# Optimization experiments

Hardware: AMD Instinct MI355X
Metric: run time of the kernel (lower is better)

The kernel has to match this reference:

```python
import jax, jax.numpy as jnp
import numpy as np

PS = 2      # patch_size
TOPK = 3    # topk


def setup_inputs() -> dict:
    key = jax.random.key(0)
    x = jax.random.normal(key, (8, 128, 64, 64), dtype=jnp.float32)
    alpha = jnp.asarray(5.0, dtype=jnp.float32)  # nn.Parameter alpha
    return {"x": x, "alpha": alpha}


def _forward(x, alpha):
    ps = PS
    b, c, h, w = x.shape
    nph, npw = h // ps, w // ps
    npatch = nph * npw
    pa = ps * ps
    # F.normalize(p=2, dim=-3) with torch eps=1e-12
    norm = jnp.maximum(jnp.sqrt(jnp.sum(x * x, axis=1, keepdims=True)), 1e-12)
    x = x / norm
    # patchify -> [b, c, npatch, patch_area] (patches h-major, pixels row-major)
    xp = x.reshape(b, c, nph, ps, npw, ps).transpose(0, 1, 2, 4, 3, 5)
    xp = xp.reshape(b, c, npatch, pa)
    diag_idx = jnp.arange(ps) * (ps + 1)  # [0, 3] for ps=2
    # gather diagonal pixels of each patch -> [b, ps, npatch, c]
    xd = xp[:, :, :, diag_idx].transpose(0, 3, 2, 1)
    # patch correlation matmul -> [b, ps, npatch, npatch]
    corr = jnp.einsum('bpnc,bpmc->bpnm', xd, xd)
    avg = jnp.mean(corr, axis=1, keepdims=True)
    s = jnp.concatenate([corr, avg], axis=1)  # [b, ps+1, npatch, npatch]
    # ZeroWindow gaussian mask (rat_s=0.05); channel index = patch center (r,c)
    sr, sc = 0.05 * nph, 0.05 * npw
    rr = jnp.arange(nph, dtype=jnp.float32)
    cc = jnp.arange(npw, dtype=jnp.float32)
    cent_r, cent_c = jnp.meshgrid(rr, cc, indexing='ij')
    cent_r = cent_r.reshape(npatch)
    cent_c = cent_c.reshape(npatch)
    gr = jnp.exp(-(rr[None, :] - cent_r[:, None]) ** 2 / (2.0 * sr * sr))  # [npatch, nph]
    gc = jnp.exp(-(cc[None, :] - cent_c[:, None]) ** 2 / (2.0 * sc * sc))  # [npatch, npw]
    mask = (1.0 - gr[:, :, None] * gc[:, None, :]).reshape(npatch, npatch)
    s = s * mask[None, None]
    a = s * alpha
    # double (row + col) softmax
    s = jax.nn.softmax(a, axis=-1) * jax.nn.softmax(a, axis=-2)
    # expand avg channel to all patch pixels, scatter diagonal channels back
    new_x = jnp.broadcast_to(s[:, -1:], (b, pa, npatch, npatch))
    new_x = new_x.at[:, diag_idx].set(s[:, :ps])
    # un-patchify second npatch axis to spatial [b, npatch, h, w]
    y = jnp.swapaxes(new_x, 1, 3)  # [b, npatch, npatch, pa]
    y = y.reshape(b, npatch, nph, npw, ps, ps).transpose(0, 1, 2, 4, 3, 5)
    y = y.reshape(b, npatch, h, w)
    # topk over the npatch axis (dim=-3)
    vals = jax.lax.top_k(jnp.moveaxis(y, 1, -1), TOPK)[0]  # [b, h, w, k]
    return jnp.moveaxis(vals, -1, 1)  # [b, k, h, w]


def reference(x, alpha):
    return _forward(x, alpha)
```

## Files before the change

### kernel.cpp

```cpp
#include <hip/hip_runtime.h>
#include <hip/hip_bf16.h>
#include <math.h>

#define NB 8
#define NC 128
#define NH 64
#define NW 64
#define NP 1024
#define TWO_SIG2 5.12f

static const size_t CORR_OFF_B = 0;
static const size_t XD_OFF_B   = (size_t)NB * 2 * NP * NP * 4;
static const size_t RSUM_OFF_B = XD_OFF_B + (size_t)NB * 2 * NP * NC * 2;

typedef __bf16 bf16x8 __attribute__((ext_vector_type(8)));
typedef float f32x4 __attribute__((ext_vector_type(4)));

__device__ __forceinline__ int iabs_(int v) { return v < 0 ? -v : v; }

#define INSERT3(v, A, Bq, Cq)                \
  {                                          \
    const float _c1 = fminf(A, (v));         \
    A = fmaxf(A, (v));                       \
    const float _c2 = fminf(Bq, _c1);        \
    Bq = fmaxf(Bq, _c1);                     \
    Cq = fmaxf(Cq, _c2);                     \
  }

#define MERGE3(a0, a1, a2, b0, b1, b2)       \
  {                                          \
    const float _x1 = fmaxf(a0, b0);         \
    const float _y1 = fminf(a0, b0);         \
    const float _x2 = fmaxf(a1, b1);         \
    const float _z  = fmaxf(a2, b2);         \
    a0 = _x1;                                \
    a1 = fmaxf(_y1, _x2);                    \
    a2 = fmaxf(fminf(_y1, _x2), _z);         \
  }

__global__ __launch_bounds__(256) void k1_norm(const float* __restrict__ x,
                                               __hip_bfloat16* __restrict__ xd) {
  __shared__ __align__(16) float tile[NC * 65];
  const int chunk = blockIdx.x;
  const int p = blockIdx.y;
  const int b = blockIdx.z;
  const int t = threadIdx.x;
  const int pix = t & 63;
  const int cw = t >> 6;
  const int nbase = chunk * 64;

  {
    const int n = nbase + pix;
    const int i = ((n >> 5) << 1) + p;
    const int j = ((n & 31) << 1) + p;
    const float* xb = x + (size_t)b * NC * NH * NW + (size_t)i * NW + j;
    for (int cc = 0; cc < 32; ++cc) {
      const int c = (cc << 2) + cw;
      tile[c * 65 + pix] = xb[(size_t)c * NH * NW];
    }
  }
  __syncthreads();

  const int lane = t & 63;
  const int w = t >> 6;
  for (int pg = 0; pg < 16; ++pg) {
    const int pixel = (pg << 2) + w;
    const float v0 = tile[lane * 65 + pixel];
    const float v1 = tile[(lane + 64) * 65 + pixel];
    float ss = v0 * v0 + v1 * v1;
#pragma unroll
    for (int m = 32; m >= 1; m >>= 1) ss += __shfl_xor(ss, m, 64);
    const float inv = 1.0f / fmaxf(sqrtf(ss), 1e-12f);
    __hip_bfloat16* xr = xd + ((size_t)((b * 2 + p) * NP) + nbase + pixel) * NC;
    xr[lane] = __float2bfloat16(v0 * inv);
    xr[lane + 64] = __float2bfloat16(v1 * inv);
  }
}

__global__ __launch_bounds__(256) void k2_corr(const ushort* __restrict__ xd,
                                               float* __restrict__ corr) {
  __shared__ __align__(16) __bf16 As[128 * 136];
  __shared__ __align__(16) __bf16 Bs[128 * 136];
  const int t = threadIdx.x;
  const int i0 = blockIdx.x << 7;
  const int j0 = blockIdx.y << 7;
  const int bp = blockIdx.z;

  const float4* ga = (const float4*)(xd + ((size_t)bp * NP + i0) * NC);
  const float4* gb = (const float4*)(xd + ((size_t)bp * NP + j0) * NC);
#pragma unroll
  for (int it = 0; it < 8; ++it) {
    const int f = (it << 8) + t;
    const int r = f >> 4;
    const int q = f & 15;
    const float4 va = ga[f];
    const float4 vb = gb[f];
    *(float4*)(&As[r * 136 + q * 8]) = va;
    *(float4*)(&Bs[r * 136 + q * 8]) = vb;
  }
  __syncthreads();

  const int wave = t >> 6;
  const int lane = t & 63;
  const int lrow = lane & 15;
  const int kq = lane >> 4;

  f32x4 acc[2][8];
#pragma unroll
  for (int rt = 0; rt < 2; ++rt)
#pragma unroll
    for (int ct = 0; ct < 8; ++ct)
#pragma unroll
      for (int u = 0; u < 4; ++u) acc[rt][ct][u] = 0.f;

#pragma unroll
  for (int kc = 0; kc < 4; ++kc) {
    const int kk = kc * 32 + (kq << 3);
    bf16x8 a[2], bfr[8];
#pragma unroll
    for (int rt = 0; rt < 2; ++rt)
      a[rt] = *(const bf16x8*)(&As[(wave * 32 + rt * 16 + lrow) * 136 + kk]);
#pragma unroll
    for (int ct = 0; ct < 8; ++ct)
      bfr[ct] = *(const bf16x8*)(&Bs[(ct * 16 + lrow) * 136 + kk]);
#pragma unroll
    for (int rt = 0; rt < 2; ++rt)
#pragma unroll
      for (int ct = 0; ct < 8; ++ct)
        acc[rt][ct] = __builtin_amdgcn_mfma_f32_16x16x32_bf16(a[rt], bfr[ct], acc[rt][ct], 0, 0, 0);
  }

  float* cb = corr + (size_t)bp * NP * NP;
#pragma unroll
  for (int rt = 0; rt < 2; ++rt) {
#pragma unroll
    for (int reg = 0; reg < 4; ++reg) {
      const int n = i0 + wave * 32 + rt * 16 + kq * 4 + reg;
      float* rowp = cb + (size_t)n * NP + j0 + lrow;
#pragma unroll
      for (int ct = 0; ct < 8; ++ct)
        rowp[ct * 16] = acc[rt][ct][reg];
    }
  }
}

__global__ __launch_bounds__(256) void k3_sums(const float* __restrict__ corr,
                                               const float* __restrict__ alpha_p,
                                               float* __restrict__ rsum) {
  __shared__ float er[32];
  const int t = threadIdx.x;
  if (t < 32) er[t] = __expf(-(float)(t * t) / TWO_SIG2);
  __syncthreads();

  const int chunk = blockIdx.x & 63;
  const int b = blockIdx.x >> 6;
  const float alpha = *alpha_p;
  const int wave = t >> 6;
  const int lane = t & 63;

  for (int rr = 0; rr < 4; ++rr) {
    const int n = chunk * 16 + wave * 4 + rr;
    const int rn = n >> 5, cn = n & 31;
    const float4* p0 = (const float4*)(corr + ((size_t)(b * 2 + 0) * NP + n) * NP);
    const float4* p1 = (const float4*)(corr + ((size_t)(b * 2 + 1) * NP + n) * NP);
    float s0 = 0.f, s1 = 0.f, s2 = 0.f;
#pragma unroll
    for (int it = 0; it < 4; ++it) {
      const int m4 = it * 64 + lane;
      const float4 v0 = p0[m4];
      const float4 v1 = p1[m4];
      float c0[4], c1[4];
      *(float4*)c0 = v0;
      *(float4*)c1 = v1;
      const int m = m4 << 2;
      const int rm = m >> 5, cm = m & 31;
      const float gr = er[iabs_(rn - rm)];
#pragma unroll
      for (int u = 0; u < 4; ++u) {
        const float g = gr * er[iabs_(cn - (cm + u))];
        const float f = alpha * (1.f - g);
        s0 += __expf(f * c0[u]);
        s1 += __expf(f * c1[u]);
        s2 += __expf(f * 0.5f * (c0[u] + c1[u]));
      }
    }
#pragma unroll
    for (int off = 32; off >= 1; off >>= 1) {
      s0 += __shfl_xor(s0, off, 64);
      s1 += __shfl_xor(s1, off, 64);
      s2 += __shfl_xor(s2, off, 64);
    }
    if (lane == 0) {
      float* rsb = rsum + (size_t)b * 3 * NP;
      rsb[n] = s0;
      rsb[NP + n] = s1;
      rsb[2 * NP + n] = s2;
    }
  }
}

__global__ __launch_bounds__(256) void k4_topk(const float* __restrict__ corr,
                                               const float* __restrict__ alpha_p,
                                               const float* __restrict__ rsum,
                                               float* __restrict__ out) {
  __shared__ float er[32];
  __shared__ float red[4][9];
  const int t = threadIdx.x;
  if (t < 32) er[t] = __expf(-(float)(t * t) / TWO_SIG2);
  __syncthreads();

  const int n = blockIdx.x & (NP - 1);
  const int b = blockIdx.x >> 10;
  const float alpha = *alpha_p;
  const int rn = n >> 5, cn = n & 31;

  const float4 v0 = ((const float4*)(corr + ((size_t)(b * 2 + 0) * NP + n) * NP))[t];
  const float4 v1 = ((const float4*)(corr + ((size_t)(b * 2 + 1) * NP + n) * NP))[t];
  const float* rsb = rsum + (size_t)b * 3 * NP;
  const float ir0 = 1.f / rsb[n];
  const float ir1 = 1.f / rsb[NP + n];
  const float ir2 = 1.f / rsb[2 * NP + n];
  const float4 w0 = ((const float4*)(rsb))[t];
  const float4 w1 = ((const float4*)(rsb + NP))[t];
  const float4 w2 = ((const float4*)(rsb + 2 * NP))[t];

  float c0[4], c1[4], s0[4], s1[4], s2[4];
  *(float4*)c0 = v0;
  *(float4*)c1 = v1;
  *(float4*)s0 = w0;
  *(float4*)s1 = w1;
  *(float4*)s2 = w2;

  float a0[3], a1[3], a2[3];
#pragma unroll
  for (int k = 0; k < 3; ++k) { a0[k] = -1e30f; a1[k] = -1e30f; a2[k] = -1e30f; }

  const int m0 = t << 2;
  const int rm = m0 >> 5;
  const int cmb = m0 & 31;
  const float gr = er[iabs_(rn - rm)];
#pragma unroll
  for (int u = 0; u < 4; ++u) {
    const float g = gr * er[iabs_(cn - (cmb + u))];
    const float f = alpha * (1.f - g);
    const float e0 = __expf(f * c0[u]);
    const float e1 = __expf(f * c1[u]);
    const float e2 = __expf(f * 0.5f * (c0[u] + c1[u]));
    const float q0 = e0 * e0 * ir0 / s0[u];
    const float q1 = e1 * e1 * ir1 / s1[u];
    const float q2 = e2 * e2 * ir2 / s2[u];
    INSERT3(q0, a0[0], a1[0], a2[0]);
    INSERT3(q1, a0[1], a1[1], a2[1]);
    INSERT3(q2, a0[2], a1[2], a2[2]);
  }

#pragma unroll
  for (int off = 1; off < 64; off <<= 1) {
#pragma unroll
    for (int k = 0; k < 3; ++k) {
      const float b0 = __shfl_xor(a0[k], off, 64);
      const float b1 = __shfl_xor(a1[k], off, 64);
      const float b2 = __shfl_xor(a2[k], off, 64);
      MERGE3(a0[k], a1[k], a2[k], b0, b1, b2);
    }
  }

  const int w = t >> 6;
  if ((t & 63) == 0) {
#pragma unroll
    for (int k = 0; k < 3; ++k) {
      red[w][k * 3 + 0] = a0[k];
      red[w][k * 3 + 1] = a1[k];
      red[w][k * 3 + 2] = a2[k];
    }
  }
  __syncthreads();

  if (t == 0) {
    float f0[3], f1[3], f2[3];
#pragma unroll
    for (int k = 0; k < 3; ++k) {
      f0[k] = red[0][k * 3 + 0];
      f1[k] = red[0][k * 3 + 1];
      f2[k] = red[0][k * 3 + 2];
      for (int ww = 1; ww < 4; ++ww) {
        const float b0 = red[ww][k * 3 + 0];
        const float b1 = red[ww][k * 3 + 1];
        const float b2 = red[ww][k * 3 + 2];
        MERGE3(f0[k], f1[k], f2[k], b0, b1, b2);
      }
    }
    float* ob = out + (size_t)b * 3 * (NH * NW);
    const int i00 = ((rn << 1) * NW) + (cn << 1);
#pragma unroll
    for (int tt = 0; tt < 3; ++tt) {
      float* op = ob + (size_t)tt * (NH * NW);
      const float r0 = (tt == 0) ? f0[0] : (tt == 1) ? f1[0] : f2[0];
      const float r1 = (tt == 0) ? f0[1] : (tt == 1) ? f1[1] : f2[1];
      const float r2 = (tt == 0) ? f0[2] : (tt == 1) ? f1[2] : f2[2];
      op[i00] = r0;
      op[i00 + NW + 1] = r1;
      op[i00 + 1] = r2;
      op[i00 + NW] = r2;
    }
  }
}

extern "C" void kernel_launch(void* const* d_in, const int* in_sizes, int n_in,
                              void* d_out, int out_size, void* d_ws, size_t ws_size,
                              hipStream_t stream) {
  const float* x = (const float*)d_in[0];
  const float* alpha = (const float*)d_in[1];
  float* out = (float*)d_out;
  char* ws = (char*)d_ws;

  float* corr = (float*)(ws + CORR_OFF_B);
  __hip_bfloat16* xd = (__hip_bfloat16*)(ws + XD_OFF_B);
  float* rsum = (float*)(ws + RSUM_OFF_B);

  k1_norm<<<dim3(16, 2, NB), 256, 0, stream>>>(x, xd);
  k2_corr<<<dim3(8, 8, NB * 2), 256, 0, stream>>>((const ushort*)xd, corr);
  k3_sums<<<dim3(NB * 64), 256, 0, stream>>>(corr, alpha, rsum);
  k4_topk<<<dim3(NB * NP), 256, 0, stream>>>(corr, alpha, rsum, out);
}
```

Before: 127.5 us.

## Fuse correlation matmul into softmax-sum and top-k kernels, recomputing instead of storing corr

Removes the materialised 64 MB fp32 correlation matrix. The MFMA matmul is now recomputed inside both the row-sum kernel and the top-k kernel, and the exp/mask epilogue is applied directly on the accumulators. Row sums are accumulated across column chunks with atomics, which needs a memset. Top-k partials per column chunk go to a small buffer that a new merge kernel reduces. The gain is far less HBM traffic, paid for with doubled matmul work and low grid parallelism (512 blocks per kernel).

After: 119.1 us. 6.6% less time.

```diff
diff --git a/kernel.cpp b/kernel.cpp
--- a/kernel.cpp
+++ b/kernel.cpp
@@ -9,9 +9,9 @@
 #define NP 1024
 #define TWO_SIG2 5.12f
 
-static const size_t CORR_OFF_B = 0;
-static const size_t XD_OFF_B   = (size_t)NB * 2 * NP * NP * 4;
-static const size_t RSUM_OFF_B = XD_OFF_B + (size_t)NB * 2 * NP * NC * 2;
+static const size_t RSUM_OFF_B = 0;
+static const size_t PBUF_OFF_B = (size_t)NB * 3 * NP * 4;
+static const size_t XD_OFF_B   = PBUF_OFF_B + (size_t)NB * NP * 3 * 4 * 3 * 4;
 
 typedef __bf16 bf16x8 __attribute__((ext_vector_type(8)));
 typedef float f32x4 __attribute__((ext_vector_type(4)));
@@ -77,232 +77,294 @@
   }
 }
 
-__global__ __launch_bounds__(256) void k2_corr(const ushort* __restrict__ xd,
-                                               float* __restrict__ corr) {
-  __shared__ __align__(16) __bf16 As[128 * 136];
-  __shared__ __align__(16) __bf16 Bs[128 * 136];
+__global__ __launch_bounds__(256) void k2_sums(const ushort* __restrict__ xd,
+                                               const float* __restrict__ alpha_p,
+                                               float* __restrict__ rsum) {
+  __shared__ __align__(16) __bf16 As[2][64 * 136];
+  __shared__ __align__(16) __bf16 Bs[2][64 * 136];
+  __shared__ float er[32];
   const int t = threadIdx.x;
-  const int i0 = blockIdx.x << 7;
-  const int j0 = blockIdx.y << 7;
-  const int bp = blockIdx.z;
-
-  const float4* ga = (const float4*)(xd + ((size_t)bp * NP + i0) * NC);
-  const float4* gb = (const float4*)(xd + ((size_t)bp * NP + j0) * NC);
-#pragma unroll
-  for (int it = 0; it < 8; ++it) {
-    const int f = (it << 8) + t;
-    const int r = f >> 4;
-    const int q = f & 15;
-    const float4 va = ga[f];
-    const float4 vb = gb[f];
-    *(float4*)(&As[r * 136 + q * 8]) = va;
-    *(float4*)(&Bs[r * 136 + q * 8]) = vb;
-  }
-  __syncthreads();
+  if (t < 32) er[t] = __expf(-(float)(t * t) / TWO_SIG2);
+
+  const int cchunk = blockIdx.x;
+  const int rowtile = blockIdx.y;
+  const int b = blockIdx.z;
+  const int i0 = rowtile << 6;
+  const int jb = cchunk << 8;
+  const float alpha = *alpha_p;
+
+#pragma unroll
+  for (int pl = 0; pl < 2; ++pl) {
+    const float4* ga = (const float4*)(xd + ((size_t)(b * 2 + pl) * NP + i0) * NC);
+#pragma unroll
+    for (int it = 0; it < 4; ++it) {
+      const int f = (it << 8) + t;
+      const int r = f >> 4, q = f & 15;
+      *(float4*)(&As[pl][r * 136 + q * 8]) = ga[f];
+    }
+  }
 
   const int wave = t >> 6;
   const int lane = t & 63;
   const int lrow = lane & 15;
   const int kq = lane >> 4;
 
-  f32x4 acc[2][8];
-#pragma unroll
-  for (int rt = 0; rt < 2; ++rt)
-#pragma unroll
-    for (int ct = 0; ct < 8; ++ct)
-#pragma unroll
-      for (int u = 0; u < 4; ++u) acc[rt][ct][u] = 0.f;
-
-#pragma unroll
-  for (int kc = 0; kc < 4; ++kc) {
-    const int kk = kc * 32 + (kq << 3);
-    bf16x8 a[2], bfr[8];
-#pragma unroll
-    for (int rt = 0; rt < 2; ++rt)
-      a[rt] = *(const bf16x8*)(&As[(wave * 32 + rt * 16 + lrow) * 136 + kk]);
-#pragma unroll
-    for (int ct = 0; ct < 8; ++ct)
-      bfr[ct] = *(const bf16x8*)(&Bs[(ct * 16 + lrow) * 136 + kk]);
-#pragma unroll
-    for (int rt = 0; rt < 2; ++rt)
-#pragma unroll
-      for (int ct = 0; ct < 8; ++ct)
-        acc[rt][ct] = __builtin_amdgcn_mfma_f32_16x16x32_bf16(a[rt], bfr[ct], acc[rt][ct], 0, 0, 0);
-  }
-
-  float* cb = corr + (size_t)bp * NP * NP;
-#pragma unroll
-  for (int rt = 0; rt < 2; ++rt) {
-#pragma unroll
-    for (int reg = 0; reg < 4; ++reg) {
-      const int n = i0 + wave * 32 + rt * 16 + kq * 4 + reg;
-      float* rowp = cb + (size_t)n * NP + j0 + lrow;
-#pragma unroll
-      for (int ct = 0; ct < 8; ++ct)
-        rowp[ct * 16] = acc[rt][ct][reg];
-    }
-  }
-}
-
-__global__ __launch_bounds__(256) void k3_sums(const float* __restrict__ corr,
+  float sums[3][4];
+#pragma unroll
+  for (int ch = 0; ch < 3; ++ch)
+#pragma unroll
+    for (int reg = 0; reg < 4; ++reg) sums[ch][reg] = 0.f;
+
+  for (int sc = 0; sc < 4; ++sc) {
+    const int j0 = jb + (sc << 6);
+    __syncthreads();
+#pragma unroll
+    for (int pl = 0; pl < 2; ++pl) {
+      const float4* gb = (const float4*)(xd + ((size_t)(b * 2 + pl) * NP + j0) * NC);
+#pragma unroll
+      for (int it = 0; it < 4; ++it) {
+        const int f = (it << 8) + t;
+        const int r = f >> 4, q = f & 15;
+        *(float4*)(&Bs[pl][r * 136 + q * 8]) = gb[f];
+      }
+    }
+    __syncthreads();
+
+    f32x4 acc[2][4];
+#pragma unroll
+    for (int pl = 0; pl < 2; ++pl)
+#pragma unroll
+      for (int ct = 0; ct < 4; ++ct)
+#pragma unroll
+        for (int u = 0; u < 4; ++u) acc[pl][ct][u] = 0.f;
+
+#pragma unroll
+    for (int kc = 0; kc < 4; ++kc) {
+      const int kk = kc * 32 + (kq << 3);
+      const bf16x8 a0 = *(const bf16x8*)(&As[0][(wave * 16 + lrow) * 136 + kk]);
+      const bf16x8 a1 = *(const bf16x8*)(&As[1][(wave * 16 + lrow) * 136 + kk]);
+#pragma unroll
+      for (int ct = 0; ct < 4; ++ct) {
+        const bf16x8 b0 = *(const bf16x8*)(&Bs[0][(ct * 16 + lrow) * 136 + kk]);
+        const bf16x8 b1 = *(const bf16x8*)(&Bs[1][(ct * 16 + lrow) * 136 + kk]);
+        acc[0][ct] = __builtin_amdgcn_mfma_f32_16x16x32_bf16(a0, b0, acc[0][ct], 0, 0, 0);
+        acc[1][ct] = __builtin_amdgcn_mfma_f32_16x16x32_bf16(a1, b1, acc[1][ct], 0, 0, 0);
+      }
+    }
+
+#pragma unroll
+    for (int ct = 0; ct < 4; ++ct) {
+      const int m = j0 + ct * 16 + lrow;
+      const int rm = m >> 5, cm = m & 31;
+#pragma unroll
+      for (int reg = 0; reg < 4; ++reg) {
+        const int n = i0 + wave * 16 + kq * 4 + reg;
+        const int rn = n >> 5, cn = n & 31;
+        const float g = er[iabs_(rn - rm)] * er[iabs_(cn - cm)];
+        const float fm = alpha * (1.f - g);
+        const float c0 = acc[0][ct][reg];
+        const float c1 = acc[1][ct][reg];
+        sums[0][reg] += __expf(fm * c0);
+        sums[1][reg] += __expf(fm * c1);
+        sums[2][reg] += __expf(fm * 0.5f * (c0 + c1));
+      }
+    }
+  }
+
+#pragma unroll
+  for (int off = 1; off < 16; off <<= 1)
+#pragma unroll
+    for (int ch = 0; ch < 3; ++ch)
+#pragma unroll
+      for (int reg = 0; reg < 4; ++reg)
+        sums[ch][reg] += __shfl_xor(sums[ch][reg], off, 64);
+
+  if (lrow == 0) {
+#pragma unroll
+    for (int ch = 0; ch < 3; ++ch)
+#pragma unroll
+      for (int reg = 0; reg < 4; ++reg) {
+        const int n = i0 + wave * 16 + kq * 4 + reg;
+        atomicAdd(&rsum[((size_t)b * 3 + ch) * NP + n], sums[ch][reg]);
+      }
+  }
+}
+
+__global__ __launch_bounds__(256) void k4_topk(const ushort* __restrict__ xd,
                                                const float* __restrict__ alpha_p,
-                                               float* __restrict__ rsum) {
+                                               const float* __restrict__ rsum,
+                                               float* __restrict__ pbuf) {
+  __shared__ __align__(16) __bf16 As[2][64 * 136];
+  __shared__ __align__(16) __bf16 Bs[2][64 * 136];
   __shared__ float er[32];
+  __shared__ float rsr[3][64];
+  __shared__ float rsc[3][256];
   const int t = threadIdx.x;
   if (t < 32) er[t] = __expf(-(float)(t * t) / TWO_SIG2);
-  __syncthreads();
-
-  const int chunk = blockIdx.x & 63;
-  const int b = blockIdx.x >> 6;
+
+  const int cchunk = blockIdx.x;
+  const int rowtile = blockIdx.y;
+  const int b = blockIdx.z;
+  const int i0 = rowtile << 6;
+  const int jb = cchunk << 8;
   const float alpha = *alpha_p;
+
+  if (t < 192) {
+    const int ch = t >> 6, r = t & 63;
+    rsr[ch][r] = 1.0f / rsum[((size_t)b * 3 + ch) * NP + i0 + r];
+  }
+#pragma unroll
+  for (int ch = 0; ch < 3; ++ch)
+    rsc[ch][t] = 1.0f / rsum[((size_t)b * 3 + ch) * NP + jb + t];
+
+#pragma unroll
+  for (int pl = 0; pl < 2; ++pl) {
+    const float4* ga = (const float4*)(xd + ((size_t)(b * 2 + pl) * NP + i0) * NC);
+#pragma unroll
+    for (int it = 0; it < 4; ++it) {
+      const int f = (it << 8) + t;
+      const int r = f >> 4, q = f & 15;
+      *(float4*)(&As[pl][r * 136 + q * 8]) = ga[f];
+    }
+  }
+
   const int wave = t >> 6;
   const int lane = t & 63;
-
-  for (int rr = 0; rr < 4; ++rr) {
-    const int n = chunk * 16 + wave * 4 + rr;
-    const int rn = n >> 5, cn = n & 31;
-    const float4* p0 = (const float4*)(corr + ((size_t)(b * 2 + 0) * NP + n) * NP);
-    const float4* p1 = (const float4*)(corr + ((size_t)(b * 2 + 1) * NP + n) * NP);
-    float s0 = 0.f, s1 = 0.f, s2 = 0.f;
-#pragma unroll
-    for (int it = 0; it < 4; ++it) {
-      const int m4 = it * 64 + lane;
-      const float4 v0 = p0[m4];
-      const float4 v1 = p1[m4];
-      float c0[4], c1[4];
-      *(float4*)c0 = v0;
-      *(float4*)c1 = v1;
-      const int m = m4 << 2;
+  const int lrow = lane & 15;
+  const int kq = lane >> 4;
+
+  float tA[3][4], tB[3][4], tC[3][4];
+#pragma unroll
+  for (int ch = 0; ch < 3; ++ch)
+#pragma unroll
+    for (int reg = 0; reg < 4; ++reg) { tA[ch][reg] = -1e30f; tB[ch][reg] = -1e30f; tC[ch][reg] = -1e30f; }
+
+  for (int sc = 0; sc < 4; ++sc) {
+    const int j0 = jb + (sc << 6);
+    __syncthreads();
+#pragma unroll
+    for (int pl = 0; pl < 2; ++pl) {
+      const float4* gb = (const float4*)(xd + ((size_t)(b * 2 + pl) * NP + j0) * NC);
+#pragma unroll
+      for (int it = 0; it < 4; ++it) {
+        const int f = (it << 8) + t;
+        const int r = f >> 4, q = f & 15;
+        *(float4*)(&Bs[pl][r * 136 + q * 8]) = gb[f];
+      }
+    }
+    __syncthreads();
+
+    f32x4 acc[2][4];
+#pragma unroll
+    for (int pl = 0; pl < 2; ++pl)
+#pragma unroll
+      for (int ct = 0; ct < 4; ++ct)
+#pragma unroll
+        for (int u = 0; u < 4; ++u) acc[pl][ct][u] = 0.f;
+
+#pragma unroll
+    for (int kc = 0; kc < 4; ++kc) {
+      const int kk = kc * 32 + (kq << 3);
+      const bf16x8 a0 = *(const bf16x8*)(&As[0][(wave * 16 + lrow) * 136 + kk]);
+      const bf16x8 a1 = *(const bf16x8*)(&As[1][(wave * 16 + lrow) * 136 + kk]);
+#pragma unroll
+      for (int ct = 0; ct < 4; ++ct) {
+        const bf16x8 b0 = *(const bf16x8*)(&Bs[0][(ct * 16 + lrow) * 136 + kk]);
+        const bf16x8 b1 = *(const bf16x8*)(&Bs[1][(ct * 16 + lrow) * 136 + kk]);
+        acc[0][ct] = __builtin_amdgcn_mfma_f32_16x16x32_bf16(a0, b0, acc[0][ct], 0, 0, 0);
+        acc[1][ct] = __builtin_amdgcn_mfma_f32_16x16x32_bf16(a1, b1, acc[1][ct], 0, 0, 0);
+      }
+    }
+
+#pragma unroll
+    for (int ct = 0; ct < 4; ++ct) {
+      const int mc = sc * 64 + ct * 16 + lrow;
+      const int m = jb + mc;
       const int rm = m >> 5, cm = m & 31;
-      const float gr = er[iabs_(rn - rm)];
-#pragma unroll
-      for (int u = 0; u < 4; ++u) {
-        const float g = gr * er[iabs_(cn - (cm + u))];
-        const float f = alpha * (1.f - g);
-        s0 += __expf(f * c0[u]);
-        s1 += __expf(f * c1[u]);
-        s2 += __expf(f * 0.5f * (c0[u] + c1[u]));
-      }
-    }
-#pragma unroll
-    for (int off = 32; off >= 1; off >>= 1) {
-      s0 += __shfl_xor(s0, off, 64);
-      s1 += __shfl_xor(s1, off, 64);
-      s2 += __shfl_xor(s2, off, 64);
-    }
-    if (lane == 0) {
-      float* rsb = rsum + (size_t)b * 3 * NP;
-      rsb[n] = s0;
-      rsb[NP + n] = s1;
-      rsb[2 * NP + n] = s2;
-    }
-  }
-}
-
-__global__ __launch_bounds__(256) void k4_topk(const float* __restrict__ corr,
-                                               const float* __restrict__ alpha_p,
-                                               const float* __restrict__ rsum,
-                                               float* __restrict__ out) {
-  __shared__ float er[32];
-  __shared__ float red[4][9];
-  const int t = threadIdx.x;
-  if (t < 32) er[t] = __expf(-(float)(t * t) / TWO_SIG2);
-  __syncthreads();
-
-  const int n = blockIdx.x & (NP - 1);
-  const int b = blockIdx.x >> 10;
-  const float alpha = *alpha_p;
+      const float im0 = rsc[0][mc], im1 = rsc[1][mc], im2 = rsc[2][mc];
+#pragma unroll
+      for (int reg = 0; reg < 4; ++reg) {
+        const int nr = wave * 16 + kq * 4 + reg;
+        const int n = i0 + nr;
+        const int rn = n >> 5, cn = n & 31;
+        const float g = er[iabs_(rn - rm)] * er[iabs_(cn - cm)];
+        const float fm = alpha * (1.f - g);
+        const float c0 = acc[0][ct][reg];
+        const float c1 = acc[1][ct][reg];
+        const float e0 = __expf(fm * c0);
+        const float e1 = __expf(fm * c1);
+        const float e2 = __expf(fm * 0.5f * (c0 + c1));
+        const float q0 = e0 * e0 * rsr[0][nr] * im0;
+        const float q1 = e1 * e1 * rsr[1][nr] * im1;
+        const float q2 = e2 * e2 * rsr[2][nr] * im2;
+        INSERT3(q0, tA[0][reg], tB[0][reg], tC[0][reg]);
+        INSERT3(q1, tA[1][reg], tB[1][reg], tC[1][reg]);
+        INSERT3(q2, tA[2][reg], tB[2][reg], tC[2][reg]);
+      }
+    }
+  }
+
+#pragma unroll
+  for (int off = 1; off < 16; off <<= 1)
+#pragma unroll
+    for (int ch = 0; ch < 3; ++ch)
+#pragma unroll
+      for (int reg = 0; reg < 4; ++reg) {
+        const float b0 = __shfl_xor(tA[ch][reg], off, 64);
+        const float b1 = __shfl_xor(tB[ch][reg], off, 64);
+        const float b2 = __shfl_xor(tC[ch][reg], off, 64);
+        MERGE3(tA[ch][reg], tB[ch][reg], tC[ch][reg], b0, b1, b2);
+      }
+
+  if (lrow == 0) {
+#pragma unroll
+    for (int ch = 0; ch < 3; ++ch)
+#pragma unroll
+      for (int reg = 0; reg < 4; ++reg) {
+        const int n = i0 + wave * 16 + kq * 4 + reg;
+        const size_t base = ((((size_t)b * NP + n) * 3 + ch) * 4 + cchunk) * 3;
+        pbuf[base + 0] = tA[ch][reg];
+        pbuf[base + 1] = tB[ch][reg];
+        pbuf[base + 2] = tC[ch][reg];
+      }
+  }
+}
+
+__global__ __launch_bounds__(256) void k5_merge(const float* __restrict__ pbuf,
+                                                float* __restrict__ out) {
+  const int tau = blockIdx.x * 256 + threadIdx.x;
+  const int b = tau >> 10;
+  const int n = tau & (NP - 1);
   const int rn = n >> 5, cn = n & 31;
 
-  const float4 v0 = ((const float4*)(corr + ((size_t)(b * 2 + 0) * NP + n) * NP))[t];
-  const float4 v1 = ((const float4*)(corr + ((size_t)(b * 2 + 1) * NP + n) * NP))[t];
-  const float* rsb = rsum + (size_t)b * 3 * NP;
-  const float ir0 = 1.f / rsb[n];
-  const float ir1 = 1.f / rsb[NP + n];
-  const float ir2 = 1.f / rsb[2 * NP + n];
-  const float4 w0 = ((const float4*)(rsb))[t];
-  const float4 w1 = ((const float4*)(rsb + NP))[t];
-  const float4 w2 = ((const float4*)(rsb + 2 * NP))[t];
-
-  float c0[4], c1[4], s0[4], s1[4], s2[4];
-  *(float4*)c0 = v0;
-  *(float4*)c1 = v1;
-  *(float4*)s0 = w0;
-  *(float4*)s1 = w1;
-  *(float4*)s2 = w2;
-
-  float a0[3], a1[3], a2[3];
-#pragma unroll
-  for (int k = 0; k < 3; ++k) { a0[k] = -1e30f; a1[k] = -1e30f; a2[k] = -1e30f; }
-
-  const int m0 = t << 2;
-  const int rm = m0 >> 5;
-  const int cmb = m0 & 31;
-  const float gr = er[iabs_(rn - rm)];
-#pragma unroll
-  for (int u = 0; u < 4; ++u) {
-    const float g = gr * er[iabs_(cn - (cmb + u))];
-    const float f = alpha * (1.f - g);
-    const float e0 = __expf(f * c0[u]);
-    const float e1 = __expf(f * c1[u]);
-    const float e2 = __expf(f * 0.5f * (c0[u] + c1[u]));
-    const float q0 = e0 * e0 * ir0 / s0[u];
-    const float q1 = e1 * e1 * ir1 / s1[u];
-    const float q2 = e2 * e2 * ir2 / s2[u];
-    INSERT3(q0, a0[0], a1[0], a2[0]);
-    INSERT3(q1, a0[1], a1[1], a2[1]);
-    INSERT3(q2, a0[2], a1[2], a2[2]);
-  }
-
-#pragma unroll
-  for (int off = 1; off < 64; off <<= 1) {
-#pragma unroll
-    for (int k = 0; k < 3; ++k) {
-      const float b0 = __shfl_xor(a0[k], off, 64);
-      const float b1 = __shfl_xor(a1[k], off, 64);
-      const float b2 = __shfl_xor(a2[k], off, 64);
-      MERGE3(a0[k], a1[k], a2[k], b0, b1, b2);
-    }
-  }
-
-  const int w = t >> 6;
-  if ((t & 63) == 0) {
-#pragma unroll
-    for (int k = 0; k < 3; ++k) {
-      red[w][k * 3 + 0] = a0[k];
-      red[w][k * 3 + 1] = a1[k];
-      red[w][k * 3 + 2] = a2[k];
-    }
-  }
-  __syncthreads();
-
-  if (t == 0) {
-    float f0[3], f1[3], f2[3];
-#pragma unroll
-    for (int k = 0; k < 3; ++k) {
-      f0[k] = red[0][k * 3 + 0];
-      f1[k] = red[0][k * 3 + 1];
-      f2[k] = red[0][k * 3 + 2];
-      for (int ww = 1; ww < 4; ++ww) {
-        const float b0 = red[ww][k * 3 + 0];
-        const float b1 = red[ww][k * 3 + 1];
-        const float b2 = red[ww][k * 3 + 2];
-        MERGE3(f0[k], f1[k], f2[k], b0, b1, b2);
-      }
-    }
-    float* ob = out + (size_t)b * 3 * (NH * NW);
-    const int i00 = ((rn << 1) * NW) + (cn << 1);
-#pragma unroll
-    for (int tt = 0; tt < 3; ++tt) {
-      float* op = ob + (size_t)tt * (NH * NW);
-      const float r0 = (tt == 0) ? f0[0] : (tt == 1) ? f1[0] : f2[0];
-      const float r1 = (tt == 0) ? f0[1] : (tt == 1) ? f1[1] : f2[1];
-      const float r2 = (tt == 0) ? f0[2] : (tt == 1) ? f1[2] : f2[2];
-      op[i00] = r0;
-      op[i00 + NW + 1] = r1;
-      op[i00 + 1] = r2;
-      op[i00 + NW] = r2;
-    }
+  float f0[3], f1[3], f2[3];
+#pragma unroll
+  for (int ch = 0; ch < 3; ++ch) {
+    const size_t base = (((size_t)tau * 3 + ch) * 4) * 3;
+    f0[ch] = pbuf[base + 0];
+    f1[ch] = pbuf[base + 1];
+    f2[ch] = pbuf[base + 2];
+#pragma unroll
+    for (int p = 1; p < 4; ++p) {
+      const float b0 = pbuf[base + p * 3 + 0];
+      const float b1 = pbuf[base + p * 3 + 1];
+      const float b2 = pbuf[base + p * 3 + 2];
+      MERGE3(f0[ch], f1[ch], f2[ch], b0, b1, b2);
+    }
+  }
+
+  float* ob = out + (size_t)b * 3 * (NH * NW);
+  const int i00 = ((rn << 1) * NW) + (cn << 1);
+#pragma unroll
+  for (int tt = 0; tt < 3; ++tt) {
+    float* op = ob + (size_t)tt * (NH * NW);
+    const float r0 = (tt == 0) ? f0[0] : (tt == 1) ? f1[0] : f2[0];
+    const float r1 = (tt == 0) ? f0[1] : (tt == 1) ? f1[1] : f2[1];
+    const float r2 = (tt == 0) ? f0[2] : (tt == 1) ? f1[2] : f2[2];
+    op[i00] = r0;
+    op[i00 + NW + 1] = r1;
+    op[i00 + 1] = r2;
+    op[i00 + NW] = r2;
   }
 }
 
@@ -314,12 +376,13 @@
   float* out = (float*)d_out;
   char* ws = (char*)d_ws;
 
-  float* corr = (float*)(ws + CORR_OFF_B);
+  float* rsum = (float*)(ws + RSUM_OFF_B);
+  float* pbuf = (float*)(ws + PBUF_OFF_B);
   __hip_bfloat16* xd = (__hip_bfloat16*)(ws + XD_OFF_B);
-  float* rsum = (float*)(ws + RSUM_OFF_B);
-
+
+  hipMemsetAsync(rsum, 0, (size_t)NB * 3 * NP * sizeof(float), stream);
   k1_norm<<<dim3(16, 2, NB), 256, 0, stream>>>(x, xd);
-  k2_corr<<<dim3(8, 8, NB * 2), 256, 0, stream>>>((const ushort*)xd, corr);
-  k3_sums<<<dim3(NB * 64), 256, 0, stream>>>(corr, alpha, rsum);
-  k4_topk<<<dim3(NB * NP), 256, 0, stream>>>(corr, alpha, rsum, out);
-}
+  k2_sums<<<dim3(4, 16, NB), 256, 0, stream>>>((const ushort*)xd, alpha, rsum);
+  k4_topk<<<dim3(4, 16, NB), 256, 0, stream>>>((const ushort*)xd, alpha, rsum, pbuf);
+  k5_merge<<<dim3(32), 256, 0, stream>>>(pbuf, out);
+}
```
